# Performance work log

Measured on AMD Instinct MI355X. Metric: run time of the kernel, lower is better.

Reference implementation:

```python
import jax, jax.numpy as jnp
import numpy as np

HID = 128
NUM_LAYERS = 3
B = 256
ND, ED, SD = 16384, 65536, 131072
NP_, EP, SP = 131072, 524288, 524288


def setup_inputs():
    key = jax.random.key(0)
    ks = jax.random.split(key, 40)
    r = lambda i, sh: jax.random.normal(ks[i], sh, jnp.float32) * 0.05
    ri = lambda i, sh, hi: jax.random.randint(ks[i], sh, 0, hi, jnp.int32)
    return {
        'drug_x': r(0, (ND, 78)),
        'prot_x': r(1, (NP_, 70)),
        'd_feature': r(2, (B, HID)),
        'p_feature': r(3, (B, HID)),
        'drug_edge_index': ri(4, (2, ED), ND),
        'drug_batch': jnp.sort(ri(5, (ND,), B)),
        'drug_sub_node': ri(6, (SD,), ND),
        'drug_sub_ind': ri(7, (SD,), ND),
        'prot_edge_index': ri(8, (2, EP), NP_),
        'prot_batch': jnp.sort(ri(9, (NP_,), B)),
        'prot_sub_node': ri(10, (SP,), NP_),
        'prot_sub_ind': ri(11, (SP,), NP_),
        'enc_Wd': r(12, (78, HID)), 'enc_bd': r(13, (HID,)),
        'enc_Wp': r(14, (70, HID)), 'enc_bp': r(15, (HID,)),
        'convW_d': r(16, (NUM_LAYERS, HID, HID)), 'convb_d': r(17, (NUM_LAYERS, HID)),
        'convW_p': r(18, (NUM_LAYERS, HID, HID)), 'convb_p': r(19, (NUM_LAYERS, HID)),
        'bng_d': jnp.ones((NUM_LAYERS, HID), jnp.float32), 'bnb_d': jnp.zeros((NUM_LAYERS, HID), jnp.float32),
        'bng_p': jnp.ones((NUM_LAYERS, HID), jnp.float32), 'bnb_p': jnp.zeros((NUM_LAYERS, HID), jnp.float32),
        'vn_emb_d': r(20, (HID,)), 'vn_emb_p': r(21, (HID,)),
        'vnW_d': r(22, (NUM_LAYERS - 1, HID, HID)), 'vnb_d': r(23, (NUM_LAYERS - 1, HID)),
        'vnW_p': r(24, (NUM_LAYERS - 1, HID, HID)), 'vnb_p': r(25, (NUM_LAYERS - 1, HID)),
        'mlpd1_W': r(26, (2 * HID, HID)), 'mlpd1_b': r(27, (HID,)),
        'mlpd1_g': jnp.ones((HID,), jnp.float32), 'mlpd1_be': jnp.zeros((HID,), jnp.float32),
        'mlpp1_W': r(28, (2 * HID, HID)), 'mlpp1_b': r(29, (HID,)),
        'mlpp1_g': jnp.ones((HID,), jnp.float32), 'mlpp1_be': jnp.zeros((HID,), jnp.float32),
    }


def _bn(x, g, b):
    # training-mode batch norm (batch statistics)
    m = jnp.mean(x, 0)
    v = jnp.var(x, 0)
    return (x - m) * jax.lax.rsqrt(v + 1e-5) * g + b


def _seg_mean(x, ids, n):
    s = jax.ops.segment_sum(x, ids, num_segments=n)
    c = jax.ops.segment_sum(jnp.ones((x.shape[0],), x.dtype), ids, num_segments=n)
    return s / jnp.maximum(c, 1.0)[:, None]


def _gcn(h, W, b, ei, n):
    # PyG GCNConv: sym-normalized A+I, then linear
    src, dst = ei[0], ei[1]
    hw = h @ W
    deg = jax.ops.segment_sum(jnp.ones((src.shape[0],), h.dtype), dst, num_segments=n) + 1.0
    nrm = jax.lax.rsqrt(deg)
    msg = hw[src] * (nrm[src] * nrm[dst])[:, None]  # [E, HID]
    return jax.ops.segment_sum(msg, dst, num_segments=n) + hw * (nrm * nrm)[:, None] + b


def _forward(fl, ints):
    (drug_x, prot_x, d_feature, p_feature, enc_Wd, enc_bd, enc_Wp, enc_bp,
     convW_d, convb_d, convW_p, convb_p, bng_d, bnb_d, bng_p, bnb_p,
     vn_emb_d, vn_emb_p, vnW_d, vnb_d, vnW_p, vnb_p,
     mlpd1_W, mlpd1_b, mlpd1_g, mlpd1_be, mlpp1_W, mlpp1_b, mlpp1_g, mlpp1_be) = fl
    (d_ei, d_batch, d_sn, d_si, p_ei, p_batch, p_sn, p_si) = ints
    Nd, Npn = drug_x.shape[0], prot_x.shape[0]
    Bn = d_feature.shape[0]
    hd = drug_x @ enc_Wd + enc_bd
    hp = prot_x @ enc_Wp + enc_bp
    # virtual node init: learned embedding + pretrained fingerprint feature
    vx_d = vn_emb_d[None, :] + d_feature  # [B, HID]
    vx_p = vn_emb_p[None, :] + p_feature
    for i in range(NUM_LAYERS):
        # virtual-node broadcast -> GCN -> BN -> ReLU (dropout off / eval)
        hd = _gcn(hd + vx_d[d_batch], convW_d[i], convb_d[i], d_ei, Nd)
        hp = _gcn(hp + vx_p[p_batch], convW_p[i], convb_p[i], p_ei, Npn)
        hd = jax.nn.relu(_bn(hd, bng_d[i], bnb_d[i]))
        hp = jax.nn.relu(_bn(hp, bng_p[i], bnb_p[i]))
        # k-hop subgraph structure extraction (scatter_mean back to nodes)
        hd_struct = _seg_mean(hd[d_sn], d_si, Nd)
        hp_struct = _seg_mean(hp[p_sn], p_si, Npn)
        if i < NUM_LAYERS - 1:
            vx_d = vx_d + jax.nn.relu((jax.ops.segment_sum(hd_struct, d_batch, num_segments=Bn) + vx_d) @ vnW_d[i] + vnb_d[i])
            vx_p = vx_p + jax.nn.relu((jax.ops.segment_sum(hp_struct, p_batch, num_segments=Bn) + vx_p) @ vnW_p[i] + vnb_p[i])
    # cross-modal sync: broadcast pooled drug info onto protein nodes & vice versa
    sync_drug = hp_struct + _seg_mean(hd_struct, d_batch, Bn)[p_batch]  # [Np, HID]
    sync_prot = hd_struct + _seg_mean(hp_struct, p_batch, Bn)[d_batch]  # [Nd, HID]
    final_drug = _bn(jnp.concatenate([_seg_mean(sync_prot, d_batch, Bn), d_feature], 1) @ mlpd1_W + mlpd1_b, mlpd1_g, mlpd1_be)
    final_prot = _bn(jnp.concatenate([_seg_mean(sync_drug, p_batch, Bn), p_feature], 1) @ mlpp1_W + mlpp1_b, mlpp1_g, mlpp1_be)
    return final_drug, final_prot


def reference(drug_x, prot_x, d_feature, p_feature, drug_edge_index, drug_batch,
              drug_sub_node, drug_sub_ind, prot_edge_index, prot_batch,
              prot_sub_node, prot_sub_ind, enc_Wd, enc_bd, enc_Wp, enc_bp,
              convW_d, convb_d, convW_p, convb_p, bng_d, bnb_d, bng_p, bnb_p,
              vn_emb_d, vn_emb_p, vnW_d, vnb_d, vnW_p, vnb_p,
              mlpd1_W, mlpd1_b, mlpd1_g, mlpd1_be, mlpp1_W, mlpp1_b, mlpp1_g, mlpp1_be):
    fl = (drug_x, prot_x, d_feature, p_feature, enc_Wd, enc_bd, enc_Wp, enc_bp,
          convW_d, convb_d, convW_p, convb_p, bng_d, bnb_d, bng_p, bnb_p,
          vn_emb_d, vn_emb_p, vnW_d, vnb_d, vnW_p, vnb_p,
          mlpd1_W, mlpd1_b, mlpd1_g, mlpd1_be, mlpp1_W, mlpp1_b, mlpp1_g, mlpp1_be)
    ints = (drug_edge_index, drug_batch, drug_sub_node, drug_sub_ind,
            prot_edge_index, prot_batch, prot_sub_node, prot_sub_ind)
    return _forward(fl, ints)
```

## Files before the change

### kernel.cpp

```cpp
#include <hip/hip_runtime.h>
#include <cstdint>
#include <cstddef>

#define HID 128
#define HB 1024
#define XB 2048

using bf16x8 = __attribute__((ext_vector_type(8))) short;
using f32x4v = __attribute__((ext_vector_type(4))) float;

static __device__ __forceinline__ unsigned short f2b(float x) {
  unsigned int u = __float_as_uint(x);
  unsigned int r = u + 0x7FFFu + ((u >> 16) & 1u);
  return (unsigned short)(r >> 16);
}
static __device__ __forceinline__ float b2f(unsigned short h) {
  return __uint_as_float(((unsigned int)h) << 16);
}
static __device__ __forceinline__ float4 b2f4(ushort4 h) {
  return make_float4(b2f(h.x), b2f(h.y), b2f(h.z), b2f(h.w));
}

static __device__ __forceinline__ int lowerb(const int* __restrict__ a, int n, int v) {
  int lo = 0, hi = n;
  while (lo < hi) { int m = (lo + hi) >> 1; if (a[m] < v) lo = m + 1; else hi = m; }
  return lo;
}

__global__ __launch_bounds__(256)
void k_prep1(const int* p_dst, int EP, int* deg_p, const int* d_dst, int ED, int* deg_d,
             const int* p_si, int SP, int* scnt_p, const int* d_si, int SD, int* scnt_d,
             const float* Xd, int Kd, unsigned short* Dhi, unsigned short* Dlo, int totD,
             const float* Xp, int Kp, unsigned short* Phi, unsigned short* Plo, int totP,
             const float* convW_d, const float* convW_p,
             const float* enc_Wd, const float* enc_Wp,
             unsigned short* WhiAll, unsigned short* WloAll,
             const float* emb_d, const float* d_feat, float* vx_d,
             const float* emb_p, const float* p_feat, float* vx_p, int vhalf) {
  const int b = blockIdx.x;
  const int tid = threadIdx.x;
  if (b < 4 * HB) {
    const int seg = b & 3, lb = b >> 2;
    const int stride = HB * 256;
    const int* idx = seg == 0 ? p_dst : seg == 1 ? d_dst : seg == 2 ? p_si : d_si;
    int* cnt = seg == 0 ? deg_p : seg == 1 ? deg_d : seg == 2 ? scnt_p : scnt_d;
    const int n = seg == 0 ? EP : seg == 1 ? ED : seg == 2 ? SP : SD;
    for (int i = lb * 256 + tid; i < n; i += stride) atomicAdd(&cnt[idx[i]], 1);
  } else if (b < 4 * HB + XB) {
    const int lb = b - 4 * HB;
    for (int i = lb * 256 + tid; i < totD + totP; i += XB * 256) {
      if (i < totD) {
        const int node = i >> 7, k = i & 127;
        const float v = (k < Kd) ? Xd[(size_t)node * Kd + k] : 0.f;
        const unsigned short hi = f2b(v);
        Dhi[i] = hi;
        Dlo[i] = f2b(v - b2f(hi));
      } else {
        const int j = i - totD;
        const int node = j >> 7, k = j & 127;
        const float v = (k < Kp) ? Xp[(size_t)node * Kp + k] : 0.f;
        const unsigned short hi = f2b(v);
        Phi[j] = hi;
        Plo[j] = f2b(v - b2f(hi));
      }
    }
  } else if (b < 4 * HB + XB + 256) {
    const int lb = b - (4 * HB + XB);
    const int seg = lb >> 5;
    const float* W;
    int K;
    if (seg < 3) { W = convW_d + (size_t)seg * HID * HID; K = 128; }
    else if (seg < 6) { W = convW_p + (size_t)(seg - 3) * HID * HID; K = 128; }
    else if (seg == 6) { W = enc_Wd; K = 78; }
    else { W = enc_Wp; K = 70; }
    unsigned short* Whi = WhiAll + (size_t)seg * HID * HID;
    unsigned short* Wlo = WloAll + (size_t)seg * HID * HID;
    for (int i = (lb & 31) * 256 + tid; i < HID * HID; i += 32 * 256) {
      const int c = i >> 7, k = i & 127;
      const float v = (k < K) ? W[k * HID + c] : 0.f;
      const unsigned short hi = f2b(v);
      Whi[i] = hi;
      Wlo[i] = f2b(v - b2f(hi));
    }
  } else {
    const int lb = b - (4 * HB + XB + 256);
    for (int i = lb * 256 + tid; i < 2 * vhalf; i += 128 * 256) {
      if (i < vhalf) vx_d[i] = emb_d[i & (HID - 1)] + d_feat[i];
      else { const int j = i - vhalf; vx_p[j] = emb_p[j & (HID - 1)] + p_feat[j]; }
    }
  }
}

__global__ void k_nrm_nb(const int* deg_d, float* nrm_d, int ND,
                         const int* deg_p, float* nrm_p, int NP,
                         const int* d_batch, float* nb_d,
                         const int* p_batch, float* nb_p, int B) {
  const int stride = gridDim.x * blockDim.x;
  const int total = ND + NP + 2 * B;
  for (int i = blockIdx.x * blockDim.x + threadIdx.x; i < total; i += stride) {
    if (i < ND) nrm_d[i] = rsqrtf((float)deg_d[i] + 1.0f);
    else if (i < ND + NP) { const int j = i - ND; nrm_p[j] = rsqrtf((float)deg_p[j] + 1.0f); }
    else if (i < ND + NP + B) {
      const int b = i - ND - NP;
      nb_d[b] = (float)(lowerb(d_batch, ND, b + 1) - lowerb(d_batch, ND, b));
    } else {
      const int b = i - ND - NP - B;
      nb_p[b] = (float)(lowerb(p_batch, NP, b + 1) - lowerb(p_batch, NP, b));
    }
  }
}

__global__ __launch_bounds__(256)
void k_scan1_all(const int* c0, int* r0, int n0, int nb0,
                 const int* c1, int* r1, int n1, int nb1,
                 const int* c2, int* r2, int n2, int nb2,
                 const int* c3, int* r3, int n3, int nb3, int* aux) {
  __shared__ int sh[256];
  int b = blockIdx.x, seg = 0;
  if (b >= nb0) { b -= nb0; seg = 1; }
  if (seg == 1 && b >= nb1) { b -= nb1; seg = 2; }
  if (seg == 2 && b >= nb2) { b -= nb2; seg = 3; }
  const int* cnt = seg == 0 ? c0 : seg == 1 ? c1 : seg == 2 ? c2 : c3;
  int* row = seg == 0 ? r0 : seg == 1 ? r1 : seg == 2 ? r2 : r3;
  const int n = seg == 0 ? n0 : seg == 1 ? n1 : seg == 2 ? n2 : n3;
  const int tid = threadIdx.x;
  const int base = b * 1024 + tid * 4;
  int v0 = base + 0 < n ? cnt[base + 0] : 0;
  int v1 = base + 1 < n ? cnt[base + 1] : 0;
  int v2 = base + 2 < n ? cnt[base + 2] : 0;
  int v3 = base + 3 < n ? cnt[base + 3] : 0;
  const int s = v0 + v1 + v2 + v3;
  sh[tid] = s;
  __syncthreads();
  for (int o = 1; o < 256; o <<= 1) {
    const int t = (tid >= o) ? sh[tid - o] : 0;
    __syncthreads();
    sh[tid] += t;
    __syncthreads();
  }
  int excl = sh[tid] - s;
  if (tid == 255) aux[seg * 256 + b] = sh[255];
  if (base + 0 < n) row[base + 0] = excl; excl += v0;
  if (base + 1 < n) row[base + 1] = excl; excl += v1;
  if (base + 2 < n) row[base + 2] = excl; excl += v2;
  if (base + 3 < n) row[base + 3] = excl;
}

__global__ __launch_bounds__(256)
void k_scan2_all(int* aux, int nb0, int nb1, int nb2, int nb3) {
  __shared__ int sh[256];
  const int seg = blockIdx.x;
  const int nb = seg == 0 ? nb0 : seg == 1 ? nb1 : seg == 2 ? nb2 : nb3;
  int* a = aux + seg * 256;
  const int tid = threadIdx.x;
  const int v = tid < nb ? a[tid] : 0;
  sh[tid] = v;
  __syncthreads();
  for (int o = 1; o < 256; o <<= 1) {
    const int t = (tid >= o) ? sh[tid - o] : 0;
    __syncthreads();
    sh[tid] += t;
    __syncthreads();
  }
  if (tid < nb) a[tid] = sh[tid] - v;
}

__global__ __launch_bounds__(256)
void k_scan3_all(int* r0, int n0, int nb0, int t0, int* r1, int n1, int nb1, int t1,
                 int* r2, int n2, int nb2, int t2, int* r3, int n3, int nb3, int t3,
                 const int* aux) {
  int b = blockIdx.x, seg = 0;
  if (b >= nb0) { b -= nb0; seg = 1; }
  if (seg == 1 && b >= nb1) { b -= nb1; seg = 2; }
  if (seg == 2 && b >= nb2) { b -= nb2; seg = 3; }
  int* row = seg == 0 ? r0 : seg == 1 ? r1 : seg == 2 ? r2 : r3;
  const int n = seg == 0 ? n0 : seg == 1 ? n1 : seg == 2 ? n2 : n3;
  const int total = seg == 0 ? t0 : seg == 1 ? t1 : seg == 2 ? t2 : t3;
  const int add = aux[seg * 256 + b];
  const int base = b * 1024 + threadIdx.x * 4;
  #pragma unroll
  for (int k = 0; k < 4; ++k)
    if (base + k < n) row[base + k] += add;
  if (b == 0 && threadIdx.x == 0) row[n] = total;
}

template<bool ENC>
static __device__ __forceinline__
void gemm_block(unsigned short* __restrict__ Bt, float* __restrict__ lstats, int lb, int tid,
                const unsigned short* __restrict__ Zhi, const unsigned short* __restrict__ Zlo,
                const unsigned short* __restrict__ Wthi, const unsigned short* __restrict__ Wtlo,
                const float* __restrict__ bias, unsigned short* __restrict__ G,
                float* __restrict__ stats_sl, int slice) {
  const int w = tid >> 6;
  const int l = tid & 63;
  const int l15 = l & 15;
  const int kb = l >> 4;

  for (int i = tid; i < 128 * 16; i += 256) {
    const int c = i >> 4, k8 = i & 15;
    *(bf16x8*)(&Bt[c * 132 + k8 * 8]) = *(const bf16x8*)(Wthi + (size_t)c * 128 + k8 * 8);
  }
  if constexpr (!ENC) lstats[tid] = 0.f;

  const int rbase = lb * 128 + w * 32 + l15;
  bf16x8 ahi[2][4], alo[2][4];
  #pragma unroll
  for (int rt = 0; rt < 2; ++rt)
    #pragma unroll
    for (int ks = 0; ks < 4; ++ks) {
      ahi[rt][ks] = *(const bf16x8*)(Zhi + (size_t)(rbase + rt * 16) * 128 + ks * 32 + kb * 8);
      alo[rt][ks] = *(const bf16x8*)(Zlo + (size_t)(rbase + rt * 16) * 128 + ks * 32 + kb * 8);
    }

  f32x4v acc[2][8];
  #pragma unroll
  for (int rt = 0; rt < 2; ++rt)
    #pragma unroll
    for (int ct = 0; ct < 8; ++ct)
      acc[rt][ct] = (f32x4v){0.f, 0.f, 0.f, 0.f};

  __syncthreads();
  #pragma unroll
  for (int ks = 0; ks < 4; ++ks) {
    #pragma unroll
    for (int ct = 0; ct < 8; ++ct) {
      const bf16x8 b = *(const bf16x8*)(&Bt[(ct * 16 + l15) * 132 + ks * 32 + kb * 8]);
      acc[0][ct] = __builtin_amdgcn_mfma_f32_16x16x32_bf16(ahi[0][ks], b, acc[0][ct], 0, 0, 0);
      acc[1][ct] = __builtin_amdgcn_mfma_f32_16x16x32_bf16(ahi[1][ks], b, acc[1][ct], 0, 0, 0);
      acc[0][ct] = __builtin_amdgcn_mfma_f32_16x16x32_bf16(alo[0][ks], b, acc[0][ct], 0, 0, 0);
      acc[1][ct] = __builtin_amdgcn_mfma_f32_16x16x32_bf16(alo[1][ks], b, acc[1][ct], 0, 0, 0);
    }
  }
  __syncthreads();

  for (int i = tid; i < 128 * 16; i += 256) {
    const int c = i >> 4, k8 = i & 15;
    *(bf16x8*)(&Bt[c * 132 + k8 * 8]) = *(const bf16x8*)(Wtlo + (size_t)c * 128 + k8 * 8);
  }
  __syncthreads();
  #pragma unroll
  for (int ks = 0; ks < 4; ++ks) {
    #pragma unroll
    for (int ct = 0; ct < 8; ++ct) {
      const bf16x8 b = *(const bf16x8*)(&Bt[(ct * 16 + l15) * 132 + ks * 32 + kb * 8]);
      acc[0][ct] = __builtin_amdgcn_mfma_f32_16x16x32_bf16(ahi[0][ks], b, acc[0][ct], 0, 0, 0);
      acc[1][ct] = __builtin_amdgcn_mfma_f32_16x16x32_bf16(ahi[1][ks], b, acc[1][ct], 0, 0, 0);
    }
  }

  float bb[8];
  if constexpr (ENC) {
    #pragma unroll
    for (int ct = 0; ct < 8; ++ct) bb[ct] = bias[ct * 16 + l15];
  }
  float csum[8], csq[8];
  #pragma unroll
  for (int ct = 0; ct < 8; ++ct) { csum[ct] = 0.f; csq[ct] = 0.f; }
  #pragma unroll
  for (int rt = 0; rt < 2; ++rt) {
    const size_t grow = (size_t)lb * 128 + w * 32 + rt * 16 + (l >> 4) * 4;
    #pragma unroll
    for (int j = 0; j < 4; ++j) {
      unsigned short* gr = G + (grow + j) * 128 + l15;
      #pragma unroll
      for (int ct = 0; ct < 8; ++ct) {
        float v = acc[rt][ct][j];
        if constexpr (ENC) v += bb[ct];
        gr[ct * 16] = f2b(v);
        if constexpr (!ENC) { csum[ct] += v; csq[ct] += v * v; }
      }
    }
  }
  if constexpr (!ENC) {
    #pragma unroll
    for (int ct = 0; ct < 8; ++ct) {
      csum[ct] += __shfl_xor(csum[ct], 16);
      csum[ct] += __shfl_xor(csum[ct], 32);
      csq[ct] += __shfl_xor(csq[ct], 16);
      csq[ct] += __shfl_xor(csq[ct], 32);
    }
    if (l < 16) {
      #pragma unroll
      for (int ct = 0; ct < 8; ++ct) {
        atomicAdd(&lstats[ct * 16 + l], csum[ct]);
        atomicAdd(&lstats[128 + ct * 16 + l], csq[ct]);
      }
    }
    __syncthreads();
    atomicAdd(&stats_sl[(size_t)slice * 256 + tid], lstats[tid]);
  }
}

__global__ __launch_bounds__(256, 2)
void k_gemm_both(const unsigned short* Zhi0, const unsigned short* Zlo0,
                 const unsigned short* Whi0, const unsigned short* Wlo0,
                 unsigned short* G0, int nbk0,
                 const unsigned short* Zhi1, const unsigned short* Zlo1,
                 const unsigned short* Whi1, const unsigned short* Wlo1,
                 unsigned short* G1, float* stats_sl) {
  __shared__ unsigned short Bt[128 * 132];
  __shared__ float lstats[256];
  const int bid = blockIdx.x;
  const bool isP = bid >= nbk0;
  const int lb = isP ? bid - nbk0 : bid;
  gemm_block<false>(Bt, lstats, lb, threadIdx.x,
                    isP ? Zhi1 : Zhi0, isP ? Zlo1 : Zlo0,
                    isP ? Whi1 : Whi0, isP ? Wlo1 : Wlo0,
                    nullptr, isP ? G1 : G0, stats_sl, (isP ? 32 : 0) + (lb & 31));
}

__global__ __launch_bounds__(256, 2)
void k_fill_enc(const unsigned short* Zhi0, const unsigned short* Zlo0,
                const unsigned short* Whi0, const unsigned short* Wlo0,
                const float* bias0, unsigned short* G0, int nG0,
                const unsigned short* Zhi1, const unsigned short* Zlo1,
                const unsigned short* Whi1, const unsigned short* Wlo1,
                const float* bias1, unsigned short* G1, int nG1,
                const int* p_src, const int* p_dst, const int* rowE_p, int* curE_p,
                int* colE_p, int EP,
                const int* d_src, const int* d_dst, const int* rowE_d, int* curE_d,
                int* colE_d, int ED,
                const int* p_sn, const int* p_si, const int* rowS_p, int* curS_p,
                int* colS_p, int SP,
                const int* d_sn, const int* d_si, const int* rowS_d, int* curS_d,
                int* colS_d, int SD) {
  __shared__ unsigned short Bt[128 * 132];
  __shared__ float lstats[256];
  const int b = blockIdx.x;
  if (b < nG0 + nG1) {
    const bool isP = b >= nG0;
    gemm_block<true>(Bt, lstats, isP ? b - nG0 : b, threadIdx.x,
                     isP ? Zhi1 : Zhi0, isP ? Zlo1 : Zlo0,
                     isP ? Whi1 : Whi0, isP ? Wlo1 : Wlo0,
                     isP ? bias1 : bias0, isP ? G1 : G0, nullptr, 0);
    return;
  }
  const int fb = b - nG0 - nG1;
  const int seg = fb & 3;
  const int lb = fb >> 2;
  const int stride = 1024 * 256;
  const int start = lb * 256 + threadIdx.x;
  if (seg == 0) {
    for (int e = start; e < EP; e += stride) {
      const int d = p_dst[e];
      colE_p[rowE_p[d] + atomicAdd(&curE_p[d], 1)] = p_src[e];
    }
  } else if (seg == 1) {
    for (int e = start; e < ED; e += stride) {
      const int d = d_dst[e];
      colE_d[rowE_d[d] + atomicAdd(&curE_d[d], 1)] = d_src[e];
    }
  } else if (seg == 2) {
    for (int j = start; j < SP; j += stride) {
      const int t = p_si[j];
      colS_p[rowS_p[t] + atomicAdd(&curS_p[t], 1)] = p_sn[j];
    }
  } else {
    for (int j = start; j < SD; j += stride) {
      const int t = d_si[j];
      colS_d[rowS_d[t] + atomicAdd(&curS_d[t], 1)] = d_sn[j];
    }
  }
}

__global__ __launch_bounds__(128)
void k_bn_scale_both(float* __restrict__ stats_sl,
                     const float* g0, const float* b0, float invN0, float* scsh0, float* zero0,
                     const float* g1, const float* b1, float invN1, float* scsh1, float* zero1,
                     int zn4) {
  const int seg = blockIdx.x;
  float* base = stats_sl + (size_t)seg * 32 * 256;
  const float* g = seg ? g1 : g0;
  const float* bb = seg ? b1 : b0;
  const float invN = seg ? invN1 : invN0;
  float* scsh = seg ? scsh1 : scsh0;
  float* zero = seg ? zero1 : zero0;
  const int c = threadIdx.x;
  float s = 0.f, ss = 0.f;
  for (int k = 0; k < 32; ++k) {
    s += base[(size_t)k * 256 + c];
    ss += base[(size_t)k * 256 + 128 + c];
    base[(size_t)k * 256 + c] = 0.f;
    base[(size_t)k * 256 + 128 + c] = 0.f;
  }
  const float m = s * invN;
  const float var = ss * invN - m * m;
  const float sc = g[c] * rsqrtf(var + 1e-5f);
  scsh[c] = sc;
  scsh[HID + c] = bb[c] - m * sc;
  const float4 z = {0.f, 0.f, 0.f, 0.f};
  for (int i = c; i < zn4; i += 128) ((float4*)zero)[i] = z;
}

template<bool HASF>
__global__ __launch_bounds__(256)
void k_agg_both(const int* rE0, const int* cE0, const unsigned short* G0,
                const float* scsh0, const int* bat0, const float* vx0, const float* nrm0,
                unsigned short* Zhi0, unsigned short* Zlo0, int nbk0,
                const int* rE1, const int* cE1, const unsigned short* G1,
                const float* scsh1, const int* bat1, const float* vx1, const float* nrm1,
                unsigned short* Zhi1, unsigned short* Zlo1) {
  const int bid = blockIdx.x;
  const bool isP = bid >= nbk0;
  const int lb = isP ? bid - nbk0 : bid;
  const int* rowp = isP ? rE1 : rE0;
  const int* colp = isP ? cE1 : cE0;
  const unsigned short* G = isP ? G1 : G0;
  const float* scsh = isP ? scsh1 : scsh0;
  const int* batch = isP ? bat1 : bat0;
  const float* vx = isP ? vx1 : vx0;
  const float* nrm = isP ? nrm1 : nrm0;
  unsigned short* Zhi = isP ? Zhi1 : Zhi0;
  unsigned short* Zlo = isP ? Zlo1 : Zlo0;

  const int tid = threadIdx.x;
  const int node = lb * 8 + (tid >> 5);
  const int c4 = tid & 31;
  float4 sc, shv;
  if constexpr (HASF) {
    sc = ((const float4*)scsh)[c4];
    shv = ((const float4*)(scsh + HID))[c4];
  }
  auto loadU = [&](int i) -> float4 {
    float4 v = b2f4(*(const ushort4*)(G + (size_t)i * HID + c4 * 4));
    if constexpr (HASF) {
      v.x = fmaxf(v.x * sc.x + shv.x, 0.f);
      v.y = fmaxf(v.y * sc.y + shv.y, 0.f);
      v.z = fmaxf(v.z * sc.z + shv.z, 0.f);
      v.w = fmaxf(v.w * sc.w + shv.w, 0.f);
    }
    const float4 u = *(const float4*)(vx + (size_t)batch[i] * HID + c4 * 4);
    v.x += u.x; v.y += u.y; v.z += u.z; v.w += u.w;
    return v;
  };
  const int lo = rowp[node], hi = rowp[node + 1];
  const float nv = nrm[node];
  const float s2 = nv * nv;
  float4 acc = loadU(node);
  acc.x *= s2; acc.y *= s2; acc.z *= s2; acc.w *= s2;
  int e = lo;
  for (; e + 4 <= hi; e += 4) {
    const int i0 = colp[e], i1 = colp[e + 1], i2 = colp[e + 2], i3 = colp[e + 3];
    const float w0 = nrm[i0] * nv, w1 = nrm[i1] * nv, w2 = nrm[i2] * nv, w3 = nrm[i3] * nv;
    const float4 v0 = loadU(i0);
    const float4 v1 = loadU(i1);
    const float4 v2 = loadU(i2);
    const float4 v3 = loadU(i3);
    acc.x += v0.x * w0 + v1.x * w1 + v2.x * w2 + v3.x * w3;
    acc.y += v0.y * w0 + v1.y * w1 + v2.y * w2 + v3.y * w3;
    acc.z += v0.z * w0 + v1.z * w1 + v2.z * w2 + v3.z * w3;
    acc.w += v0.w * w0 + v1.w * w1 + v2.w * w2 + v3.w * w3;
  }
  for (; e < hi; ++e) {
    const int i0 = colp[e];
    const float w = nrm[i0] * nv;
    const float4 v = loadU(i0);
    acc.x += v.x * w; acc.y += v.y * w; acc.z += v.z * w; acc.w += v.w * w;
  }
  ushort4 h, lo4;
  h.x = f2b(acc.x); lo4.x = f2b(acc.x - b2f(h.x));
  h.y = f2b(acc.y); lo4.y = f2b(acc.y - b2f(h.y));
  h.z = f2b(acc.z); lo4.z = f2b(acc.z - b2f(h.z));
  h.w = f2b(acc.w); lo4.w = f2b(acc.w - b2f(h.w));
  *(ushort4*)(Zhi + (size_t)node * HID + c4 * 4) = h;
  *(ushort4*)(Zlo + (size_t)node * HID + c4 * 4) = lo4;
}

__global__ __launch_bounds__(256)
void k_sub_pool_both(const int* rS0, const int* cS0, const unsigned short* G0, const float* scsh0,
                     const int* bat0, float* sumS0, int nbk0,
                     const int* rS1, const int* cS1, const unsigned short* G1, const float* scsh1,
                     const int* bat1, float* sumS1) {
  __shared__ float sh[8][HID];
  __shared__ int batl[8];
  const int bid = blockIdx.x;
  const bool isP = bid >= nbk0;
  const int lb = isP ? bid - nbk0 : bid;
  const int* rowp = isP ? rS1 : rS0;
  const int* colp = isP ? cS1 : cS0;
  const unsigned short* G = isP ? G1 : G0;
  const float* scsh = isP ? scsh1 : scsh0;
  const int* batch = isP ? bat1 : bat0;
  float* sumS = isP ? sumS1 : sumS0;

  const int tid = threadIdx.x;
  const int grp = tid >> 5;
  const int node = lb * 8 + grp;
  const int c4 = tid & 31;
  const float4 sc = ((const float4*)scsh)[c4];
  const float4 shv = ((const float4*)(scsh + HID))[c4];
  const int lo = rowp[node], hi = rowp[node + 1];
  float4 acc = {0.f, 0.f, 0.f, 0.f};
  int e = lo;
  for (; e + 4 <= hi; e += 4) {
    const int i0 = colp[e], i1 = colp[e + 1], i2 = colp[e + 2], i3 = colp[e + 3];
    const float4 v0 = b2f4(*(const ushort4*)(G + (size_t)i0 * HID + c4 * 4));
    const float4 v1 = b2f4(*(const ushort4*)(G + (size_t)i1 * HID + c4 * 4));
    const float4 v2 = b2f4(*(const ushort4*)(G + (size_t)i2 * HID + c4 * 4));
    const float4 v3 = b2f4(*(const ushort4*)(G + (size_t)i3 * HID + c4 * 4));
    acc.x += fmaxf(v0.x * sc.x + shv.x, 0.f) + fmaxf(v1.x * sc.x + shv.x, 0.f)
           + fmaxf(v2.x * sc.x + shv.x, 0.f) + fmaxf(v3.x * sc.x + shv.x, 0.f);
    acc.y += fmaxf(v0.y * sc.y + shv.y, 0.f) + fmaxf(v1.y * sc.y + shv.y, 0.f)
           + fmaxf(v2.y * sc.y + shv.y, 0.f) + fmaxf(v3.y * sc.y + shv.y, 0.f);
    acc.z += fmaxf(v0.z * sc.z + shv.z, 0.f) + fmaxf(v1.z * sc.z + shv.z, 0.f)
           + fmaxf(v2.z * sc.z + shv.z, 0.f) + fmaxf(v3.z * sc.z + shv.z, 0.f);
    acc.w += fmaxf(v0.w * sc.w + shv.w, 0.f) + fmaxf(v1.w * sc.w + shv.w, 0.f)
           + fmaxf(v2.w * sc.w + shv.w, 0.f) + fmaxf(v3.w * sc.w + shv.w, 0.f);
  }
  for (; e < hi; ++e) {
    const float4 v = b2f4(*(const ushort4*)(G + (size_t)colp[e] * HID + c4 * 4));
    acc.x += fmaxf(v.x * sc.x + shv.x, 0.f);
    acc.y += fmaxf(v.y * sc.y + shv.y, 0.f);
    acc.z += fmaxf(v.z * sc.z + shv.z, 0.f);
// ... 82 lines not shown
  fpre[(size_t)gb * HID + c] = acc;
}

__global__ __launch_bounds__(256)
void k_bn_stats_both(const float* __restrict__ fpre, float* __restrict__ statsF, int B) {
  __shared__ float sh[2][256];
  const int seg = blockIdx.x >= 128 ? 1 : 0;
  const int lb = blockIdx.x - seg * 128;
  const float* X = fpre + (size_t)seg * B * HID;
  float* stats = statsF + seg * 256;
  const int tid = threadIdx.x;
  const int c = tid & (HID - 1);
  const int half = tid >> 7;
  float s = 0.f, ss = 0.f;
  for (int r = lb * 2 + half; r < B; r += 256) {
    const float v = X[(size_t)r * HID + c];
    s += v; ss += v * v;
  }
  sh[0][tid] = s; sh[1][tid] = ss;
  __syncthreads();
  if (tid < HID) {
    atomicAdd(&stats[c], sh[0][tid] + sh[0][tid + 128]);
    atomicAdd(&stats[HID + c], sh[1][tid] + sh[1][tid + 128]);
  }
}

__global__ void k_bn_apply_both(const float* __restrict__ fpre, float* __restrict__ out,
                                const float* __restrict__ statsF,
                                const float* g0, const float* b0,
                                const float* g1, const float* b1, int B, float invN) {
  const int stride = gridDim.x * blockDim.x;
  const int n4 = 2 * B * 32;
  for (int i = blockIdx.x * blockDim.x + threadIdx.x; i < n4; i += stride) {
    const int seg = i >= B * 32 ? 1 : 0;
    const int c4 = i & 31;
    const float* stats = statsF + seg * 256;
    const float4 m4 = ((const float4*)stats)[c4];
    const float4 q4 = ((const float4*)stats)[32 + c4];
    const float4 g4 = ((const float4*)(seg ? g1 : g0))[c4];
    const float4 b4 = ((const float4*)(seg ? b1 : b0))[c4];
    float4 v = ((const float4*)fpre)[i];
    float m, va;
    m = m4.x * invN; va = q4.x * invN - m * m; v.x = (v.x - m) * rsqrtf(va + 1e-5f) * g4.x + b4.x;
    m = m4.y * invN; va = q4.y * invN - m * m; v.y = (v.y - m) * rsqrtf(va + 1e-5f) * g4.y + b4.y;
    m = m4.z * invN; va = q4.z * invN - m * m; v.z = (v.z - m) * rsqrtf(va + 1e-5f) * g4.z + b4.z;
    m = m4.w * invN; va = q4.w * invN - m * m; v.w = (v.w - m) * rsqrtf(va + 1e-5f) * g4.w + b4.w;
    ((float4*)out)[i] = v;
  }
}

extern "C" void kernel_launch(void* const* d_in, const int* in_sizes, int n_in,
                              void* d_out, int out_size, void* d_ws, size_t ws_size,
                              hipStream_t stream) {
  const float* drug_x   = (const float*)d_in[0];
  const float* prot_x   = (const float*)d_in[1];
  const float* d_feat   = (const float*)d_in[2];
  const float* p_feat   = (const float*)d_in[3];
  const int*   d_ei     = (const int*)d_in[4];
  const int*   d_batch  = (const int*)d_in[5];
  const int*   d_sn     = (const int*)d_in[6];
  const int*   d_si     = (const int*)d_in[7];
  const int*   p_ei     = (const int*)d_in[8];
  const int*   p_batch  = (const int*)d_in[9];
  const int*   p_sn     = (const int*)d_in[10];
  const int*   p_si     = (const int*)d_in[11];
  const float* enc_Wd   = (const float*)d_in[12];
  const float* enc_bd   = (const float*)d_in[13];
  const float* enc_Wp   = (const float*)d_in[14];
  const float* enc_bp   = (const float*)d_in[15];
  const float* convW_d  = (const float*)d_in[16];
  const float* convW_p  = (const float*)d_in[18];
  const float* bng_d    = (const float*)d_in[20];
  const float* bnb_d    = (const float*)d_in[21];
  const float* bng_p    = (const float*)d_in[22];
  const float* bnb_p    = (const float*)d_in[23];
  const float* vn_emb_d = (const float*)d_in[24];
  const float* vn_emb_p = (const float*)d_in[25];
  const float* vnW_d    = (const float*)d_in[26];
  const float* vnb_d    = (const float*)d_in[27];
  const float* vnW_p    = (const float*)d_in[28];
  const float* vnb_p    = (const float*)d_in[29];
  const float* mlpd1_W  = (const float*)d_in[30];
  const float* mlpd1_b  = (const float*)d_in[31];
  const float* mlpd1_g  = (const float*)d_in[32];
  const float* mlpd1_be = (const float*)d_in[33];
  const float* mlpp1_W  = (const float*)d_in[34];
  const float* mlpp1_b  = (const float*)d_in[35];
  const float* mlpp1_g  = (const float*)d_in[36];
  const float* mlpp1_be = (const float*)d_in[37];

  const int ND = in_sizes[5];
  const int ED = in_sizes[4] / 2;
  const int SD = in_sizes[6];
  const int NP = in_sizes[9];
  const int EP = in_sizes[8] / 2;
  const int SP = in_sizes[10];
  const int B  = in_sizes[2] / HID;
  (void)n_in; (void)out_size; (void)ws_size;

  char* wsb = (char*)d_ws;
  size_t off = 0;
  auto alloc = [&](size_t bytes) -> void* {
    void* p = (void*)(wsb + off);
    off = (off + bytes + 255) & ~(size_t)255;
    return p;
  };
  unsigned short* Gp = (unsigned short*)alloc((size_t)NP * HID * 2);
  unsigned short* Zhi_p = (unsigned short*)alloc((size_t)NP * HID * 2);
  unsigned short* Zlo_p = (unsigned short*)alloc((size_t)NP * HID * 2);
  unsigned short* Gd = (unsigned short*)alloc((size_t)ND * HID * 2);
  unsigned short* Zhi_d = (unsigned short*)alloc((size_t)ND * HID * 2);
  unsigned short* Zlo_d = (unsigned short*)alloc((size_t)ND * HID * 2);
  unsigned short* WhiAll = (unsigned short*)alloc((size_t)8 * HID * HID * 2);
  unsigned short* WloAll = (unsigned short*)alloc((size_t)8 * HID * HID * 2);
  float* nrm_p = (float*)alloc((size_t)NP * 4);
  float* nrm_d = (float*)alloc((size_t)ND * 4);
  int* rowE_p = (int*)alloc((size_t)(NP + 1) * 4);
  int* rowE_d = (int*)alloc((size_t)(ND + 1) * 4);
  int* rowS_p = (int*)alloc((size_t)(NP + 1) * 4);
  int* rowS_d = (int*)alloc((size_t)(ND + 1) * 4);
  int* colE_p = (int*)alloc((size_t)EP * 4);
  int* colE_d = (int*)alloc((size_t)ED * 4);
  int* colS_p = (int*)alloc((size_t)SP * 4);
  int* colS_d = (int*)alloc((size_t)SD * 4);
  int* aux    = (int*)alloc(4 * 256 * 4);
  float* vx_d  = (float*)alloc((size_t)B * HID * 4);
  float* vx_p  = (float*)alloc((size_t)B * HID * 4);
  float* sum_Sd = (float*)alloc((size_t)B * HID * 4);
  float* sum_Sp = (float*)alloc((size_t)B * HID * 4);
  float* A_d   = (float*)alloc((size_t)B * HID * 4);
  float* A_p   = (float*)alloc((size_t)B * HID * 4);
  float* nb_d  = (float*)alloc((size_t)B * 4);
  float* nb_p  = (float*)alloc((size_t)B * 4);
  float* scsh_d = (float*)alloc(2 * HID * 4);
  float* scsh_p = (float*)alloc(2 * HID * 4);
  float* fpre  = (float*)alloc((size_t)2 * B * HID * 4);
  float* statsF = (float*)alloc(2 * 256 * 4);
  const size_t zstart = off;
  int* deg_p  = (int*)alloc((size_t)NP * 4);
  int* deg_d  = (int*)alloc((size_t)ND * 4);
  int* scnt_p = (int*)alloc((size_t)NP * 4);
  int* scnt_d = (int*)alloc((size_t)ND * 4);
  int* curE_p = (int*)alloc((size_t)NP * 4);
  int* curE_d = (int*)alloc((size_t)ND * 4);
  int* curS_p = (int*)alloc((size_t)NP * 4);
  int* curS_d = (int*)alloc((size_t)ND * 4);
  float* stats_sl = (float*)alloc((size_t)64 * 256 * 4);
  const size_t zend = off;

  const int* d_src = d_ei;  const int* d_dst = d_ei + ED;
  const int* p_src = p_ei;  const int* p_dst = p_ei + EP;

  hipMemsetAsync(wsb + zstart, 0, zend - zstart, stream);
  k_prep1<<<4 * HB + XB + 256 + 128, 256, 0, stream>>>(
      p_dst, EP, deg_p, d_dst, ED, deg_d, p_si, SP, scnt_p, d_si, SD, scnt_d,
      drug_x, 78, Zhi_d, Zlo_d, ND * HID, prot_x, 70, Zhi_p, Zlo_p, NP * HID,
      convW_d, convW_p, enc_Wd, enc_Wp, WhiAll, WloAll,
      vn_emb_d, d_feat, vx_d, vn_emb_p, p_feat, vx_p, B * HID);
  k_nrm_nb<<<1024, 256, 0, stream>>>(deg_d, nrm_d, ND, deg_p, nrm_p, NP,
                                     d_batch, nb_d, p_batch, nb_p, B);
  const int nbP = (NP + 1023) / 1024, nbD = (ND + 1023) / 1024;
  k_scan1_all<<<2 * nbP + 2 * nbD, 256, 0, stream>>>(
      deg_p, rowE_p, NP, nbP, deg_d, rowE_d, ND, nbD,
      scnt_p, rowS_p, NP, nbP, scnt_d, rowS_d, ND, nbD, aux);
  k_scan2_all<<<4, 256, 0, stream>>>(aux, nbP, nbD, nbP, nbD);
  k_scan3_all<<<2 * nbP + 2 * nbD, 256, 0, stream>>>(
      rowE_p, NP, nbP, EP, rowE_d, ND, nbD, ED,
      rowS_p, NP, nbP, SP, rowS_d, ND, nbD, SD, aux);

  const int nG0 = ND / 128, nG1 = NP / 128;
  k_fill_enc<<<nG0 + nG1 + 4096, 256, 0, stream>>>(
      Zhi_d, Zlo_d, WhiAll + (size_t)6 * HID * HID, WloAll + (size_t)6 * HID * HID,
      enc_bd, Gd, nG0,
      Zhi_p, Zlo_p, WhiAll + (size_t)7 * HID * HID, WloAll + (size_t)7 * HID * HID,
      enc_bp, Gp, nG1,
      p_src, p_dst, rowE_p, curE_p, colE_p, EP,
      d_src, d_dst, rowE_d, curE_d, colE_d, ED,
      p_sn, p_si, rowS_p, curS_p, colS_p, SP,
      d_sn, d_si, rowS_d, curS_d, colS_d, SD);

  for (int l = 0; l < 3; ++l) {
    if (l == 0)
      k_agg_both<false><<<ND / 8 + NP / 8, 256, 0, stream>>>(
          rowE_d, colE_d, Gd, nullptr, d_batch, vx_d, nrm_d, Zhi_d, Zlo_d, ND / 8,
          rowE_p, colE_p, Gp, nullptr, p_batch, vx_p, nrm_p, Zhi_p, Zlo_p);
    else
      k_agg_both<true><<<ND / 8 + NP / 8, 256, 0, stream>>>(
          rowE_d, colE_d, Gd, scsh_d, d_batch, vx_d, nrm_d, Zhi_d, Zlo_d, ND / 8,
          rowE_p, colE_p, Gp, scsh_p, p_batch, vx_p, nrm_p, Zhi_p, Zlo_p);
    k_gemm_both<<<ND / 128 + NP / 128, 256, 0, stream>>>(
        Zhi_d, Zlo_d, WhiAll + (size_t)l * HID * HID, WloAll + (size_t)l * HID * HID,
        Gd, ND / 128,
        Zhi_p, Zlo_p, WhiAll + (size_t)(3 + l) * HID * HID, WloAll + (size_t)(3 + l) * HID * HID,
        Gp, stats_sl);
    k_bn_scale_both<<<2, 128, 0, stream>>>(stats_sl,
        bng_d + l * HID, bnb_d + l * HID, 1.0f / (float)ND, scsh_d, sum_Sd,
        bng_p + l * HID, bnb_p + l * HID, 1.0f / (float)NP, scsh_p, sum_Sp,
        B * HID / 4);
    k_sub_pool_both<<<ND / 8 + NP / 8, 256, 0, stream>>>(
        rowS_d, colS_d, Gd, scsh_d, d_batch, sum_Sd, ND / 8,
        rowS_p, colS_p, Gp, scsh_p, p_batch, sum_Sp);
    if (l < 2)
      k_vn_update_both<<<2 * B, 128, 0, stream>>>(
          sum_Sd, vx_d, vnW_d + (size_t)l * HID * HID, vnb_d + l * HID,
          sum_Sp, vx_p, vnW_p + (size_t)l * HID * HID, vnb_p + l * HID, B);
  }

  k_final_A<<<B, 128, 0, stream>>>(sum_Sd, sum_Sp, nb_d, nb_p, A_d, A_p);
  k_final_mlp_both<<<2 * B, 128, 0, stream>>>(A_d, d_feat, mlpd1_W, mlpd1_b,
                                              A_p, p_feat, mlpp1_W, mlpp1_b, fpre, B);
  hipMemsetAsync(statsF, 0, 2 * 256 * 4, stream);
  k_bn_stats_both<<<256, 256, 0, stream>>>(fpre, statsF, B);
  k_bn_apply_both<<<128, 256, 0, stream>>>(fpre, (float*)d_out, statsF,
                                           mlpd1_g, mlpd1_be, mlpp1_g, mlpp1_be,
                                           B, 1.0f / (float)B);
}
```

Measured before the change: 720.7 us.

## Fuse input split-bf16 conversion into encoder GEMM and separate CSR fill kernel

Removes the prep-stage pass that converted drug_x/prot_x into padded hi/lo bf16 buffers. The encoder GEMM now reads the fp32 inputs directly and splits them into hi/lo in registers, which avoids writing and re-reading the intermediate arrays. The CSR fill work is moved out of the combined encoder kernel into its own launch, so the GEMM and the fill no longer share one grid. The direct loads are scalar, strided reads of rows with 78 or 70 elements, which are less coalesced than the previous vector loads.

```diff
diff --git a/kernel.cpp b/kernel.cpp
--- a/kernel.cpp
+++ b/kernel.cpp
@@ -4,7 +4,6 @@
 
 #define HID 128
 #define HB 1024
-#define XB 2048
 
 using bf16x8 = __attribute__((ext_vector_type(8))) short;
 using f32x4v = __attribute__((ext_vector_type(4))) float;
@@ -30,8 +29,6 @@
 __global__ __launch_bounds__(256)
 void k_prep1(const int* p_dst, int EP, int* deg_p, const int* d_dst, int ED, int* deg_d,
              const int* p_si, int SP, int* scnt_p, const int* d_si, int SD, int* scnt_d,
-             const float* Xd, int Kd, unsigned short* Dhi, unsigned short* Dlo, int totD,
-             const float* Xp, int Kp, unsigned short* Phi, unsigned short* Plo, int totP,
              const float* convW_d, const float* convW_p,
              const float* enc_Wd, const float* enc_Wp,
              unsigned short* WhiAll, unsigned short* WloAll,
@@ -46,26 +43,8 @@
     int* cnt = seg == 0 ? deg_p : seg == 1 ? deg_d : seg == 2 ? scnt_p : scnt_d;
     const int n = seg == 0 ? EP : seg == 1 ? ED : seg == 2 ? SP : SD;
     for (int i = lb * 256 + tid; i < n; i += stride) atomicAdd(&cnt[idx[i]], 1);
-  } else if (b < 4 * HB + XB) {
+  } else if (b < 4 * HB + 256) {
     const int lb = b - 4 * HB;
-    for (int i = lb * 256 + tid; i < totD + totP; i += XB * 256) {
-      if (i < totD) {
-        const int node = i >> 7, k = i & 127;
-        const float v = (k < Kd) ? Xd[(size_t)node * Kd + k] : 0.f;
-        const unsigned short hi = f2b(v);
-        Dhi[i] = hi;
-        Dlo[i] = f2b(v - b2f(hi));
-      } else {
-        const int j = i - totD;
-        const int node = j >> 7, k = j & 127;
-        const float v = (k < Kp) ? Xp[(size_t)node * Kp + k] : 0.f;
-        const unsigned short hi = f2b(v);
-        Phi[j] = hi;
-        Plo[j] = f2b(v - b2f(hi));
-      }
-    }
-  } else if (b < 4 * HB + XB + 256) {
-    const int lb = b - (4 * HB + XB);
     const int seg = lb >> 5;
     const float* W;
     int K;
@@ -83,7 +62,7 @@
       Wlo[i] = f2b(v - b2f(hi));
     }
   } else {
-    const int lb = b - (4 * HB + XB + 256);
+    const int lb = b - (4 * HB + 256);
     for (int i = lb * 256 + tid; i < 2 * vhalf; i += 128 * 256) {
       if (i < vhalf) vx_d[i] = emb_d[i & (HID - 1)] + d_feat[i];
       else { const int j = i - vhalf; vx_p[j] = emb_p[j & (HID - 1)] + p_feat[j]; }
@@ -184,110 +163,38 @@
   if (b == 0 && threadIdx.x == 0) row[n] = total;
 }
 
-template<bool ENC>
-static __device__ __forceinline__
-void gemm_block(unsigned short* __restrict__ Bt, float* __restrict__ lstats, int lb, int tid,
-                const unsigned short* __restrict__ Zhi, const unsigned short* __restrict__ Zlo,
-                const unsigned short* __restrict__ Wthi, const unsigned short* __restrict__ Wtlo,
-                const float* __restrict__ bias, unsigned short* __restrict__ G,
-                float* __restrict__ stats_sl, int slice) {
-  const int w = tid >> 6;
-  const int l = tid & 63;
-  const int l15 = l & 15;
-  const int kb = l >> 4;
-
-  for (int i = tid; i < 128 * 16; i += 256) {
-    const int c = i >> 4, k8 = i & 15;
-    *(bf16x8*)(&Bt[c * 132 + k8 * 8]) = *(const bf16x8*)(Wthi + (size_t)c * 128 + k8 * 8);
-  }
-  if constexpr (!ENC) lstats[tid] = 0.f;
-
-  const int rbase = lb * 128 + w * 32 + l15;
-  bf16x8 ahi[2][4], alo[2][4];
-  #pragma unroll
-  for (int rt = 0; rt < 2; ++rt)
-    #pragma unroll
-    for (int ks = 0; ks < 4; ++ks) {
-      ahi[rt][ks] = *(const bf16x8*)(Zhi + (size_t)(rbase + rt * 16) * 128 + ks * 32 + kb * 8);
-      alo[rt][ks] = *(const bf16x8*)(Zlo + (size_t)(rbase + rt * 16) * 128 + ks * 32 + kb * 8);
-    }
-
-  f32x4v acc[2][8];
-  #pragma unroll
-  for (int rt = 0; rt < 2; ++rt)
-    #pragma unroll
-    for (int ct = 0; ct < 8; ++ct)
-      acc[rt][ct] = (f32x4v){0.f, 0.f, 0.f, 0.f};
-
-  __syncthreads();
-  #pragma unroll
-  for (int ks = 0; ks < 4; ++ks) {
-    #pragma unroll
-    for (int ct = 0; ct < 8; ++ct) {
-      const bf16x8 b = *(const bf16x8*)(&Bt[(ct * 16 + l15) * 132 + ks * 32 + kb * 8]);
-      acc[0][ct] = __builtin_amdgcn_mfma_f32_16x16x32_bf16(ahi[0][ks], b, acc[0][ct], 0, 0, 0);
-      acc[1][ct] = __builtin_amdgcn_mfma_f32_16x16x32_bf16(ahi[1][ks], b, acc[1][ct], 0, 0, 0);
-      acc[0][ct] = __builtin_amdgcn_mfma_f32_16x16x32_bf16(alo[0][ks], b, acc[0][ct], 0, 0, 0);
-      acc[1][ct] = __builtin_amdgcn_mfma_f32_16x16x32_bf16(alo[1][ks], b, acc[1][ct], 0, 0, 0);
-    }
-  }
-  __syncthreads();
-
-  for (int i = tid; i < 128 * 16; i += 256) {
-    const int c = i >> 4, k8 = i & 15;
-    *(bf16x8*)(&Bt[c * 132 + k8 * 8]) = *(const bf16x8*)(Wtlo + (size_t)c * 128 + k8 * 8);
-  }
-  __syncthreads();
-  #pragma unroll
-  for (int ks = 0; ks < 4; ++ks) {
-    #pragma unroll
-    for (int ct = 0; ct < 8; ++ct) {
-      const bf16x8 b = *(const bf16x8*)(&Bt[(ct * 16 + l15) * 132 + ks * 32 + kb * 8]);
-      acc[0][ct] = __builtin_amdgcn_mfma_f32_16x16x32_bf16(ahi[0][ks], b, acc[0][ct], 0, 0, 0);
-      acc[1][ct] = __builtin_amdgcn_mfma_f32_16x16x32_bf16(ahi[1][ks], b, acc[1][ct], 0, 0, 0);
-    }
-  }
-
-  float bb[8];
-  if constexpr (ENC) {
-    #pragma unroll
-    for (int ct = 0; ct < 8; ++ct) bb[ct] = bias[ct * 16 + l15];
-  }
-  float csum[8], csq[8];
-  #pragma unroll
-  for (int ct = 0; ct < 8; ++ct) { csum[ct] = 0.f; csq[ct] = 0.f; }
-  #pragma unroll
-  for (int rt = 0; rt < 2; ++rt) {
-    const size_t grow = (size_t)lb * 128 + w * 32 + rt * 16 + (l >> 4) * 4;
-    #pragma unroll
-    for (int j = 0; j < 4; ++j) {
-      unsigned short* gr = G + (grow + j) * 128 + l15;
-      #pragma unroll
-      for (int ct = 0; ct < 8; ++ct) {
-        float v = acc[rt][ct][j];
-        if constexpr (ENC) v += bb[ct];
-        gr[ct * 16] = f2b(v);
-        if constexpr (!ENC) { csum[ct] += v; csq[ct] += v * v; }
-      }
-    }
-  }
-  if constexpr (!ENC) {
-    #pragma unroll
-    for (int ct = 0; ct < 8; ++ct) {
-      csum[ct] += __shfl_xor(csum[ct], 16);
-      csum[ct] += __shfl_xor(csum[ct], 32);
-      csq[ct] += __shfl_xor(csq[ct], 16);
-      csq[ct] += __shfl_xor(csq[ct], 32);
-    }
-    if (l < 16) {
-      #pragma unroll
-      for (int ct = 0; ct < 8; ++ct) {
-        atomicAdd(&lstats[ct * 16 + l], csum[ct]);
-        atomicAdd(&lstats[128 + ct * 16 + l], csq[ct]);
-      }
-    }
-    __syncthreads();
-    atomicAdd(&stats_sl[(size_t)slice * 256 + tid], lstats[tid]);
+__global__ void k_fill_all(const int* p_src, const int* p_dst, const int* rowE_p, int* curE_p,
+                           int* colE_p, int EP,
+                           const int* d_src, const int* d_dst, const int* rowE_d, int* curE_d,
+                           int* colE_d, int ED,
+                           const int* p_sn, const int* p_si, const int* rowS_p, int* curS_p,
+                           int* colS_p, int SP,
+                           const int* d_sn, const int* d_si, const int* rowS_d, int* curS_d,
+                           int* colS_d, int SD) {
+  const int seg = blockIdx.x & 3;
+  const int lb = blockIdx.x >> 2;
+  const int stride = (gridDim.x >> 2) * blockDim.x;
+  const int start = lb * blockDim.x + threadIdx.x;
+  if (seg == 0) {
+    for (int e = start; e < EP; e += stride) {
+      const int d = p_dst[e];
+      colE_p[rowE_p[d] + atomicAdd(&curE_p[d], 1)] = p_src[e];
+    }
+  } else if (seg == 1) {
+    for (int e = start; e < ED; e += stride) {
+      const int d = d_dst[e];
+      colE_d[rowE_d[d] + atomicAdd(&curE_d[d], 1)] = d_src[e];
+    }
+  } else if (seg == 2) {
+    for (int j = start; j < SP; j += stride) {
+      const int t = p_si[j];
+      colS_p[rowS_p[t] + atomicAdd(&curS_p[t], 1)] = p_sn[j];
+    }
+  } else {
+    for (int j = start; j < SD; j += stride) {
+      const int t = d_si[j];
+      colS_d[rowS_d[t] + atomicAdd(&curS_d[t], 1)] = d_sn[j];
+    }
   }
 }
 
@@ -303,62 +210,202 @@
   const int bid = blockIdx.x;
   const bool isP = bid >= nbk0;
   const int lb = isP ? bid - nbk0 : bid;
-  gemm_block<false>(Bt, lstats, lb, threadIdx.x,
-                    isP ? Zhi1 : Zhi0, isP ? Zlo1 : Zlo0,
-                    isP ? Whi1 : Whi0, isP ? Wlo1 : Wlo0,
-                    nullptr, isP ? G1 : G0, stats_sl, (isP ? 32 : 0) + (lb & 31));
+  const unsigned short* Zhi = isP ? Zhi1 : Zhi0;
+  const unsigned short* Zlo = isP ? Zlo1 : Zlo0;
+  const unsigned short* Wthi = isP ? Whi1 : Whi0;
+  const unsigned short* Wtlo = isP ? Wlo1 : Wlo0;
+  unsigned short* G = isP ? G1 : G0;
+  const int slice = (isP ? 32 : 0) + (lb & 31);
+
+  const int tid = threadIdx.x;
+  const int w = tid >> 6;
+  const int l = tid & 63;
+  const int l15 = l & 15;
+  const int kb = l >> 4;
+
+  for (int i = tid; i < 128 * 16; i += 256) {
+    const int c = i >> 4, k8 = i & 15;
+    *(bf16x8*)(&Bt[c * 132 + k8 * 8]) = *(const bf16x8*)(Wthi + (size_t)c * 128 + k8 * 8);
+  }
+  lstats[tid] = 0.f;
+
+  const int rbase = lb * 128 + w * 32 + l15;
+  bf16x8 ahi[2][4], alo[2][4];
+  #pragma unroll
+  for (int rt = 0; rt < 2; ++rt)
+    #pragma unroll
+    for (int ks = 0; ks < 4; ++ks) {
+      ahi[rt][ks] = *(const bf16x8*)(Zhi + (size_t)(rbase + rt * 16) * 128 + ks * 32 + kb * 8);
+      alo[rt][ks] = *(const bf16x8*)(Zlo + (size_t)(rbase + rt * 16) * 128 + ks * 32 + kb * 8);
+    }
+
+  f32x4v acc[2][8];
+  #pragma unroll
+  for (int rt = 0; rt < 2; ++rt)
+    #pragma unroll
+    for (int ct = 0; ct < 8; ++ct)
+      acc[rt][ct] = (f32x4v){0.f, 0.f, 0.f, 0.f};
+
+  __syncthreads();
+  #pragma unroll
+  for (int ks = 0; ks < 4; ++ks) {
+    #pragma unroll
+    for (int ct = 0; ct < 8; ++ct) {
+      const bf16x8 b = *(const bf16x8*)(&Bt[(ct * 16 + l15) * 132 + ks * 32 + kb * 8]);
+      acc[0][ct] = __builtin_amdgcn_mfma_f32_16x16x32_bf16(ahi[0][ks], b, acc[0][ct], 0, 0, 0);
+      acc[1][ct] = __builtin_amdgcn_mfma_f32_16x16x32_bf16(ahi[1][ks], b, acc[1][ct], 0, 0, 0);
+      acc[0][ct] = __builtin_amdgcn_mfma_f32_16x16x32_bf16(alo[0][ks], b, acc[0][ct], 0, 0, 0);
+      acc[1][ct] = __builtin_amdgcn_mfma_f32_16x16x32_bf16(alo[1][ks], b, acc[1][ct], 0, 0, 0);
+    }
+  }
+  __syncthreads();
+
+  for (int i = tid; i < 128 * 16; i += 256) {
+    const int c = i >> 4, k8 = i & 15;
+    *(bf16x8*)(&Bt[c * 132 + k8 * 8]) = *(const bf16x8*)(Wtlo + (size_t)c * 128 + k8 * 8);
+  }
+  __syncthreads();
+  #pragma unroll
+  for (int ks = 0; ks < 4; ++ks) {
+    #pragma unroll
+    for (int ct = 0; ct < 8; ++ct) {
+      const bf16x8 b = *(const bf16x8*)(&Bt[(ct * 16 + l15) * 132 + ks * 32 + kb * 8]);
+      acc[0][ct] = __builtin_amdgcn_mfma_f32_16x16x32_bf16(ahi[0][ks], b, acc[0][ct], 0, 0, 0);
+      acc[1][ct] = __builtin_amdgcn_mfma_f32_16x16x32_bf16(ahi[1][ks], b, acc[1][ct], 0, 0, 0);
+    }
+  }
+
+  float csum[8], csq[8];
+  #pragma unroll
+  for (int ct = 0; ct < 8; ++ct) { csum[ct] = 0.f; csq[ct] = 0.f; }
+  #pragma unroll
+  for (int rt = 0; rt < 2; ++rt) {
+    const size_t grow = (size_t)lb * 128 + w * 32 + rt * 16 + (l >> 4) * 4;
+    #pragma unroll
+    for (int j = 0; j < 4; ++j) {
+      unsigned short* gr = G + (grow + j) * 128 + l15;
+      #pragma unroll
+      for (int ct = 0; ct < 8; ++ct) {
+        const float v = acc[rt][ct][j];
+        gr[ct * 16] = f2b(v);
+        csum[ct] += v;
+        csq[ct] += v * v;
+      }
+    }
+  }
+  #pragma unroll
+  for (int ct = 0; ct < 8; ++ct) {
+    csum[ct] += __shfl_xor(csum[ct], 16);
+    csum[ct] += __shfl_xor(csum[ct], 32);
+    csq[ct] += __shfl_xor(csq[ct], 16);
+    csq[ct] += __shfl_xor(csq[ct], 32);
+  }
+  if (l < 16) {
+    #pragma unroll
+    for (int ct = 0; ct < 8; ++ct) {
+      atomicAdd(&lstats[ct * 16 + l], csum[ct]);
+      atomicAdd(&lstats[128 + ct * 16 + l], csq[ct]);
+    }
+  }
+  __syncthreads();
+  atomicAdd(&stats_sl[(size_t)slice * 256 + tid], lstats[tid]);
 }
 
 __global__ __launch_bounds__(256, 2)
-void k_fill_enc(const unsigned short* Zhi0, const unsigned short* Zlo0,
-                const unsigned short* Whi0, const unsigned short* Wlo0,
-                const float* bias0, unsigned short* G0, int nG0,
-                const unsigned short* Zhi1, const unsigned short* Zlo1,
-                const unsigned short* Whi1, const unsigned short* Wlo1,
-                const float* bias1, unsigned short* G1, int nG1,
-                const int* p_src, const int* p_dst, const int* rowE_p, int* curE_p,
-                int* colE_p, int EP,
-                const int* d_src, const int* d_dst, const int* rowE_d, int* curE_d,
-                int* colE_d, int ED,
-                const int* p_sn, const int* p_si, const int* rowS_p, int* curS_p,
-                int* colS_p, int SP,
-                const int* d_sn, const int* d_si, const int* rowS_d, int* curS_d,
-                int* colS_d, int SD) {
+void k_gemm_enc_direct(const float* X0, int K0,
+                       const unsigned short* Whi0, const unsigned short* Wlo0,
+                       const float* bias0, unsigned short* G0, int nbk0,
+                       const float* X1, int K1,
+                       const unsigned short* Whi1, const unsigned short* Wlo1,
+                       const float* bias1, unsigned short* G1) {
   __shared__ unsigned short Bt[128 * 132];
-  __shared__ float lstats[256];
-  const int b = blockIdx.x;
-  if (b < nG0 + nG1) {
-    const bool isP = b >= nG0;
-    gemm_block<true>(Bt, lstats, isP ? b - nG0 : b, threadIdx.x,
-                     isP ? Zhi1 : Zhi0, isP ? Zlo1 : Zlo0,
-                     isP ? Whi1 : Whi0, isP ? Wlo1 : Wlo0,
-                     isP ? bias1 : bias0, isP ? G1 : G0, nullptr, 0);
-    return;
-  }
-  const int fb = b - nG0 - nG1;
-  const int seg = fb & 3;
-  const int lb = fb >> 2;
-  const int stride = 1024 * 256;
-  const int start = lb * 256 + threadIdx.x;
-  if (seg == 0) {
-    for (int e = start; e < EP; e += stride) {
-      const int d = p_dst[e];
-      colE_p[rowE_p[d] + atomicAdd(&curE_p[d], 1)] = p_src[e];
-    }
-  } else if (seg == 1) {
-    for (int e = start; e < ED; e += stride) {
-      const int d = d_dst[e];
-      colE_d[rowE_d[d] + atomicAdd(&curE_d[d], 1)] = d_src[e];
-    }
-  } else if (seg == 2) {
-    for (int j = start; j < SP; j += stride) {
-      const int t = p_si[j];
-      colS_p[rowS_p[t] + atomicAdd(&curS_p[t], 1)] = p_sn[j];
-    }
-  } else {
-    for (int j = start; j < SD; j += stride) {
-      const int t = d_si[j];
-      colS_d[rowS_d[t] + atomicAdd(&curS_d[t], 1)] = d_sn[j];
+  const int bid = blockIdx.x;
+  const bool isP = bid >= nbk0;
+  const int lb = isP ? bid - nbk0 : bid;
+  const float* X = isP ? X1 : X0;
+  const int K = isP ? K1 : K0;
+  const unsigned short* Wthi = isP ? Whi1 : Whi0;
+  const unsigned short* Wtlo = isP ? Wlo1 : Wlo0;
+  const float* bias = isP ? bias1 : bias0;
+  unsigned short* G = isP ? G1 : G0;
+
+  const int tid = threadIdx.x;
+  const int w = tid >> 6;
+  const int l = tid & 63;
+  const int l15 = l & 15;
+  const int kb = l >> 4;
+
+  for (int i = tid; i < 128 * 16; i += 256) {
+    const int c = i >> 4, k8 = i & 15;
+    *(bf16x8*)(&Bt[c * 132 + k8 * 8]) = *(const bf16x8*)(Wthi + (size_t)c * 128 + k8 * 8);
+  }
+
+  const int rbase = lb * 128 + w * 32 + l15;
+  bf16x8 ahi[2][4], alo[2][4];
+  #pragma unroll
+  for (int rt = 0; rt < 2; ++rt) {
+    const float* xr = X + (size_t)(rbase + rt * 16) * K;
+    #pragma unroll
+    for (int ks = 0; ks < 4; ++ks) {
+      #pragma unroll
+      for (int j = 0; j < 8; ++j) {
+        const int k = ks * 32 + kb * 8 + j;
+        const float v = (k < K) ? xr[k] : 0.f;
+        const unsigned short hi = f2b(v);
+        ahi[rt][ks][j] = (short)hi;
+        alo[rt][ks][j] = (short)f2b(v - b2f(hi));
+      }
+    }
+  }
+
+  f32x4v acc[2][8];
+  #pragma unroll
+  for (int rt = 0; rt < 2; ++rt)
+    #pragma unroll
+    for (int ct = 0; ct < 8; ++ct)
+      acc[rt][ct] = (f32x4v){0.f, 0.f, 0.f, 0.f};
+
+  __syncthreads();
+  #pragma unroll
+  for (int ks = 0; ks < 4; ++ks) {
+    #pragma unroll
+    for (int ct = 0; ct < 8; ++ct) {
+      const bf16x8 b = *(const bf16x8*)(&Bt[(ct * 16 + l15) * 132 + ks * 32 + kb * 8]);
+      acc[0][ct] = __builtin_amdgcn_mfma_f32_16x16x32_bf16(ahi[0][ks], b, acc[0][ct], 0, 0, 0);
+      acc[1][ct] = __builtin_amdgcn_mfma_f32_16x16x32_bf16(ahi[1][ks], b, acc[1][ct], 0, 0, 0);
+      acc[0][ct] = __builtin_amdgcn_mfma_f32_16x16x32_bf16(alo[0][ks], b, acc[0][ct], 0, 0, 0);
+      acc[1][ct] = __builtin_amdgcn_mfma_f32_16x16x32_bf16(alo[1][ks], b, acc[1][ct], 0, 0, 0);
+    }
+  }
+  __syncthreads();
+
+  for (int i = tid; i < 128 * 16; i += 256) {
+    const int c = i >> 4, k8 = i & 15;
+    *(bf16x8*)(&Bt[c * 132 + k8 * 8]) = *(const bf16x8*)(Wtlo + (size_t)c * 128 + k8 * 8);
+  }
+  __syncthreads();
+  #pragma unroll
+  for (int ks = 0; ks < 4; ++ks) {
+    #pragma unroll
+    for (int ct = 0; ct < 8; ++ct) {
+      const bf16x8 b = *(const bf16x8*)(&Bt[(ct * 16 + l15) * 132 + ks * 32 + kb * 8]);
+      acc[0][ct] = __builtin_amdgcn_mfma_f32_16x16x32_bf16(ahi[0][ks], b, acc[0][ct], 0, 0, 0);
+      acc[1][ct] = __builtin_amdgcn_mfma_f32_16x16x32_bf16(ahi[1][ks], b, acc[1][ct], 0, 0, 0);
+    }
+  }
+
+  float bb[8];
+  #pragma unroll
+  for (int ct = 0; ct < 8; ++ct) bb[ct] = bias[ct * 16 + l15];
+  #pragma unroll
+  for (int rt = 0; rt < 2; ++rt) {
+    const size_t grow = (size_t)lb * 128 + w * 32 + rt * 16 + (l >> 4) * 4;
+    #pragma unroll
+    for (int j = 0; j < 4; ++j) {
+      unsigned short* gr = G + (grow + j) * 128 + l15;
+      #pragma unroll
+      for (int ct = 0; ct < 8; ++ct)
+        gr[ct * 16] = f2b(acc[rt][ct][j] + bb[ct]);
     }
   }
 }
@@ -747,9 +794,8 @@
   const int* p_src = p_ei;  const int* p_dst = p_ei + EP;
 
   hipMemsetAsync(wsb + zstart, 0, zend - zstart, stream);
-  k_prep1<<<4 * HB + XB + 256 + 128, 256, 0, stream>>>(
+  k_prep1<<<4 * HB + 256 + 128, 256, 0, stream>>>(
       p_dst, EP, deg_p, d_dst, ED, deg_d, p_si, SP, scnt_p, d_si, SD, scnt_d,
-      drug_x, 78, Zhi_d, Zlo_d, ND * HID, prot_x, 70, Zhi_p, Zlo_p, NP * HID,
       convW_d, convW_p, enc_Wd, enc_Wp, WhiAll, WloAll,
       vn_emb_d, d_feat, vx_d, vn_emb_p, p_feat, vx_p, B * HID);
   k_nrm_nb<<<1024, 256, 0, stream>>>(deg_d, nrm_d, ND, deg_p, nrm_p, NP,
@@ -762,17 +808,17 @@
   k_scan3_all<<<2 * nbP + 2 * nbD, 256, 0, stream>>>(
       rowE_p, NP, nbP, EP, rowE_d, ND, nbD, ED,
       rowS_p, NP, nbP, SP, rowS_d, ND, nbD, SD, aux);
-
-  const int nG0 = ND / 128, nG1 = NP / 128;
-  k_fill_enc<<<nG0 + nG1 + 4096, 256, 0, stream>>>(
-      Zhi_d, Zlo_d, WhiAll + (size_t)6 * HID * HID, WloAll + (size_t)6 * HID * HID,
-      enc_bd, Gd, nG0,
-      Zhi_p, Zlo_p, WhiAll + (size_t)7 * HID * HID, WloAll + (size_t)7 * HID * HID,
-      enc_bp, Gp, nG1,
+  k_fill_all<<<4096, 256, 0, stream>>>(
       p_src, p_dst, rowE_p, curE_p, colE_p, EP,
       d_src, d_dst, rowE_d, curE_d, colE_d, ED,
       p_sn, p_si, rowS_p, curS_p, colS_p, SP,
       d_sn, d_si, rowS_d, curS_d, colS_d, SD);
+
+  k_gemm_enc_direct<<<ND / 128 + NP / 128, 256, 0, stream>>>(
+      drug_x, 78, WhiAll + (size_t)6 * HID * HID, WloAll + (size_t)6 * HID * HID,
+      enc_bd, Gd, ND / 128,
+      prot_x, 70, WhiAll + (size_t)7 * HID * HID, WloAll + (size_t)7 * HID * HID,
+      enc_bp, Gp);
 
   for (int l = 0; l < 3; ++l) {
     if (l == 0)
```

Result: faster. 628.7 us (-12.8%).
